# Kernel optimization log

Hardware: AMD Instinct MI355X
Metric: run time of the kernel (lower is better)

Reference implementation:

```python
import jax, jax.numpy as jnp
import numpy as np
import math

BATCH, NODES, IN_DIM = 8, 2048, 64
HEADS, OUT_DIM = 4, 32
D = HEADS * OUT_DIM
N_NEIGHBORS = 32


def setup_inputs() -> dict:
    key = jax.random.key(0)
    ks = jax.random.split(key, 6)
    s = lambda fan: 1.0 / np.sqrt(fan)
    return {
        "x": jax.random.normal(ks[0], (BATCH, NODES, IN_DIM), jnp.float32),
        "Wq": jax.random.normal(ks[1], (D, IN_DIM), jnp.float32) * s(IN_DIM),
        "bq": jnp.zeros((D,), jnp.float32),
        "Wk": jax.random.normal(ks[2], (D, IN_DIM), jnp.float32) * s(IN_DIM),
        "bk": jnp.zeros((D,), jnp.float32),
        "mlp_w": jax.random.normal(ks[3], (HEADS, HEADS), jnp.float32) * s(HEADS),
        "mlp_b": jnp.zeros((HEADS,), jnp.float32),
        "ln_g": jnp.ones((NODES,), jnp.float32),
        "ln_b": jnp.zeros((NODES,), jnp.float32),
    }


def _layernorm(x, g, b, eps=1e-5):
    m = x.mean(-1, keepdims=True)
    v = x.var(-1, keepdims=True)
    return (x - m) * jax.lax.rsqrt(v + eps) * g + b


def _forward(x, Wq, bq, Wk, bk, mlp_w, mlp_b, ln_g, ln_b):
    B, N, _ = x.shape
    # static graph branch (computed in the original forward, but its result is
    # never used in the returned adjacency -- kept for fidelity; DCE'd under jit)
    adj_static = jax.nn.softmax(
        jax.nn.relu(_layernorm(jnp.einsum('bnc,bmc->bnm', x, x), ln_g, ln_b)), axis=1)
    del adj_static

    q = x @ Wq.T + bq  # (B,N,D)
    k = x @ Wk.T + bk
    # (B,D,N) -> (B,H,d,N)
    q = q.transpose(0, 2, 1).reshape(B, HEADS, OUT_DIM, N)
    k = k.transpose(0, 2, 1).reshape(B, HEADS, OUT_DIM, N)
    q = q.transpose(0, 1, 3, 2)  # (B,H,N,d)

    # torch.split(query, chunk, dim=-1) splits q over out_dim, k over nodes; zip
    # truncates to the shorter list -> only min(nq,nk) chunks are processed.
    chunk = math.ceil(N / 2)
    nq = math.ceil(OUT_DIM / chunk)
    nk = math.ceil(N / chunk)
    inv_sqrt_d = jnp.float32(1.0 / math.sqrt(OUT_DIM))
    outs = []
    for i in range(min(nq, nk)):
        qc = q[..., i * chunk:(i + 1) * chunk]          # (B,H,N,dc)
        kc = k[..., i * chunk:(i + 1) * chunk]          # (B,H,d,Uc)
        a = jnp.einsum('bhnd,bhdu->bhnu', qc, kc) * inv_sqrt_d
        # dropout is identity in eval mode; soft-threshold with beta=0
        a = jnp.sign(a) * jax.nn.relu(jnp.abs(a))
        # 1x1 conv over head channels + relu, residual add
        a = jax.nn.relu(jnp.einsum('oh,bhnu->bonu', mlp_w, a)
                        + mlp_b[None, :, None, None]) + a
        outs.append(a)
    attn = jnp.concatenate(outs, axis=-1)               # (B,H,N,U)

    scores = attn.sum(axis=1)                           # (B,N,U)
    vals, idx = jax.lax.top_k(scores, N_NEIGHBORS)      # sorted, largest
    adj = jnp.zeros((B, N, N), x.dtype)
    bi = jnp.arange(B)[:, None, None]
    ni = jnp.arange(N)[None, :, None]
    return adj.at[bi, ni, idx].add(vals)


def reference(x, Wq, bq, Wk, bk, mlp_w, mlp_b, ln_g, ln_b):
    return _forward(x, Wq, bq, Wk, bk, mlp_w, mlp_b, ln_g, ln_b)
```

## Files before the change

kernel.cpp:

```cpp
#include <hip/hip_runtime.h>
#include <cstdint>
#include <cstddef>

#define BATCH 8
#define NODES 2048
#define IN_DIM 64
#define DTOT 128
#define NKEY 1024
#define LDK 136

typedef _Float16 half8v __attribute__((ext_vector_type(8)));
typedef float float4v __attribute__((ext_vector_type(4)));

__device__ __forceinline__ unsigned long long make_key(float v, int idx) {
    unsigned u = __float_as_uint(v);
    u = (u & 0x80000000u) ? ~u : (u | 0x80000000u);
    return ((unsigned long long)u << 32) | (unsigned)(1023 - idx);
}

__global__ __launch_bounds__(256) void proj_qk(
    const float* __restrict__ x, const float* __restrict__ Wq, const float* __restrict__ bq,
    const float* __restrict__ Wk, const float* __restrict__ bk,
    _Float16* __restrict__ qh, _Float16* __restrict__ ql,
    _Float16* __restrict__ kh, _Float16* __restrict__ kl)
{
    __shared__ float xs[64 * 68];
    __shared__ float wsh[64 * 68];

    const int t = threadIdx.x;
    const int blk = blockIdx.x;
    const int b = blk / 96;
    const int idx = blk - b * 96;

    const float* W; const float* bias;
    _Float16* oh; _Float16* ol;
    int nbase, cbase; size_t orow;
    if (idx < 64) {
        int nt = idx >> 1, ct = idx & 1;
        nbase = nt * 64; cbase = ct * 64;
        W = Wq; bias = bq; oh = qh; ol = ql;
        orow = (size_t)(b * NODES + nbase);
    } else {
        int i2 = idx - 64;
        int nt = i2 >> 1, ct = i2 & 1;
        nbase = nt * 64; cbase = ct * 64;
        W = Wk; bias = bk; oh = kh; ol = kl;
        orow = (size_t)(b * NKEY + nbase);
    }

    #pragma unroll
    for (int rep = 0; rep < 4; ++rep) {
        int f = rep * 256 + t;
        int r = f >> 4, d4 = f & 15;
        float4 xv = *(const float4*)(x + ((size_t)(b * NODES + nbase + r)) * IN_DIM + d4 * 4);
        *(float4*)(xs + r * 68 + d4 * 4) = xv;
        float4 wv = *(const float4*)(W + (size_t)(cbase + r) * IN_DIM + d4 * 4);
        *(float4*)(wsh + r * 68 + d4 * 4) = wv;
    }
    __syncthreads();

    const int w = t >> 6, l = t & 63;
    const int n_sel = w * 4 + (l >> 4);
    const int ul = l & 15;

    float acc[4][4];
    #pragma unroll
    for (int i = 0; i < 4; ++i)
        #pragma unroll
        for (int j = 0; j < 4; ++j) acc[i][j] = 0.f;

    #pragma unroll
    for (int d4 = 0; d4 < 16; ++d4) {
        float4 xv[4], wv[4];
        #pragma unroll
        for (int i = 0; i < 4; ++i)
            xv[i] = *(const float4*)(xs + (n_sel * 4 + i) * 68 + d4 * 4);
        #pragma unroll
        for (int j = 0; j < 4; ++j)
            wv[j] = *(const float4*)(wsh + (j * 16 + ul) * 68 + d4 * 4);
        #pragma unroll
        for (int i = 0; i < 4; ++i)
            #pragma unroll
            for (int j = 0; j < 4; ++j)
                acc[i][j] += xv[i].x * wv[j].x + xv[i].y * wv[j].y +
                             xv[i].z * wv[j].z + xv[i].w * wv[j].w;
    }

    #pragma unroll
    for (int j = 0; j < 4; ++j) {
        float bv = bias[cbase + j * 16 + ul];
        #pragma unroll
        for (int i = 0; i < 4; ++i) {
            float a = acc[i][j] + bv;
            _Float16 hi = (_Float16)a;
            size_t p = (orow + n_sel * 4 + i) * DTOT + cbase + j * 16 + ul;
            oh[p] = hi;
            ol[p] = (_Float16)(a - (float)hi);
        }
    }
}

__global__ __launch_bounds__(256, 4) void scores_mfma(
    const _Float16* __restrict__ qh, const _Float16* __restrict__ ql,
    const _Float16* __restrict__ kh, const _Float16* __restrict__ kl,
    const float* __restrict__ mlpw, const float* __restrict__ mlpb,
    float* __restrict__ adj)
{
    __shared__ _Float16 khs[64 * LDK];
    __shared__ _Float16 kls[64 * LDK];

    const int t = threadIdx.x;
    const int blk = blockIdx.x;
    const int b = blk >> 9;
    const int rem = blk & 511;
    const int nb = (rem >> 4) * 64;
    const int ub = (rem & 15) * 64;

    const int w = t >> 6, l = t & 63;
    const int quad = l >> 4, lane16 = l & 15;

    const size_t arow = (size_t)(b * NODES + nb + w * 16 + lane16);
    half8v Ah[4], Al[4];
    #pragma unroll
    for (int h = 0; h < 4; ++h) {
        Ah[h] = *(const half8v*)(qh + arow * DTOT + h * 32 + quad * 8);
        Al[h] = *(const half8v*)(ql + arow * DTOT + h * 32 + quad * 8);
    }

    #pragma unroll
    for (int rep = 0; rep < 4; ++rep) {
        int f = rep * 256 + t;
        int r = f >> 4, c = f & 15;
        size_t src = ((size_t)(b * NKEY + ub + r)) * DTOT + c * 8;
        *(half8v*)(&khs[r * LDK + c * 8]) = *(const half8v*)(kh + src);
        *(half8v*)(&kls[r * LDK + c * 8]) = *(const half8v*)(kl + src);
    }
    __syncthreads();

    float mw[4][4], mb4[4];
    #pragma unroll
    for (int o = 0; o < 4; ++o) {
        mb4[o] = mlpb[o];
        #pragma unroll
        for (int h = 0; h < 4; ++h) mw[o][h] = mlpw[o * 4 + h];
    }
    const float INV = 0.17677669529663687f;

    #pragma unroll
    for (int ut = 0; ut < 4; ++ut) {
        half8v Bh[4], Bl[4];
        #pragma unroll
        for (int h = 0; h < 4; ++h) {
            Bh[h] = *(const half8v*)(&khs[(ut * 16 + lane16) * LDK + h * 32 + quad * 8]);
            Bl[h] = *(const half8v*)(&kls[(ut * 16 + lane16) * LDK + h * 32 + quad * 8]);
        }
        float4v C[4];
        #pragma unroll
        for (int h = 0; h < 4; ++h) {
            float4v c = {0.f, 0.f, 0.f, 0.f};
            c = __builtin_amdgcn_mfma_f32_16x16x32_f16(Ah[h], Bh[h], c, 0, 0, 0);
            c = __builtin_amdgcn_mfma_f32_16x16x32_f16(Ah[h], Bl[h], c, 0, 0, 0);
            c = __builtin_amdgcn_mfma_f32_16x16x32_f16(Al[h], Bh[h], c, 0, 0, 0);
            C[h] = c;
        }
        #pragma unroll
        for (int r = 0; r < 4; ++r) {
            float a0 = C[0][r] * INV, a1 = C[1][r] * INV;
            float a2 = C[2][r] * INV, a3 = C[3][r] * INV;
            float ssum = a0 + a1 + a2 + a3;
            #pragma unroll
            for (int o = 0; o < 4; ++o) {
                float to = mw[o][0] * a0 + mw[o][1] * a1 + mw[o][2] * a2 + mw[o][3] * a3 + mb4[o];
                ssum += fmaxf(to, 0.f);
            }
            const size_t rowp = ((size_t)(b * NODES + nb + w * 16 + quad * 4 + r)) * NODES + NKEY;
            adj[rowp + ub + ut * 16 + lane16] = ssum;
        }
    }
}

__global__ __launch_bounds__(256) void topk_write(float* __restrict__ adj)
{
    __shared__ float scrow[4][1024];
    __shared__ unsigned long long cand[4][64];
    __shared__ float maxb[4][64];

    const int t = threadIdx.x;
    const int blk = blockIdx.x;
    const int b = blk >> 9;
    const int r0 = (blk & 511) * 4;
    const int w = t >> 6, l = t & 63;

    const int n = r0 + w;
    float* rowptr = adj + ((size_t)(b * NODES + n)) * NODES;
    const float4* S4 = (const float4*)(rowptr + NKEY);

    float4 vv[4];
    #pragma unroll
    for (int jj = 0; jj < 4; ++jj) vv[jj] = S4[jj * 64 + l];

    float m = vv[0].x;
    #pragma unroll
    for (int jj = 0; jj < 4; ++jj) {
        m = fmaxf(m, vv[jj].x); m = fmaxf(m, vv[jj].y);
        m = fmaxf(m, vv[jj].z); m = fmaxf(m, vv[jj].w);
    }

    maxb[w][l] = m;
    __builtin_amdgcn_wave_barrier();
    int r = 0;
    #pragma unroll
    for (int j = 0; j < 64; ++j) r += (maxb[w][j] > m) ? 1 : 0;
    float sel = (r <= 31) ? m : 3.4e38f;
    #pragma unroll
    for (int off = 1; off < 64; off <<= 1)
        sel = fminf(sel, __shfl_xor(sel, off, 64));
    const float T = sel;

    cand[w][l] = 0ull;
    __builtin_amdgcn_wave_barrier();
    int total = 0;
    #pragma unroll
    for (int jj = 0; jj < 4; ++jj) {
        #pragma unroll
        for (int e = 0; e < 4; ++e) {
            float v = (e == 0) ? vv[jj].x : (e == 1) ? vv[jj].y : (e == 2) ? vv[jj].z : vv[jj].w;
            bool p = (v >= T);
            unsigned long long msk = __ballot(p);
            if (p) {
                int pos = total + __popcll(msk & ((1ull << l) - 1ull));
                if (pos < 64) cand[w][pos] = make_key(v, jj * 256 + l * 4 + e);
            }
            total += (int)__popcll(msk);
        }
    }
    __builtin_amdgcn_wave_barrier();

    bool win = false; float wval = 0.f; int widx = 0;
    if (total <= 64) {
        unsigned long long key = cand[w][l];
        int r2 = 0;
        #pragma unroll
        for (int j = 0; j < 64; ++j) r2 += (cand[w][j] > key) ? 1 : 0;
        if (key != 0ull && r2 < 32) {
            win = true;
            unsigned hi = (unsigned)(key >> 32);
            wval = __uint_as_float((hi & 0x80000000u) ? (hi & 0x7fffffffu) : ~hi);
            widx = 1023 - (int)(key & 0xffffffffu);
        }
    } else {
        float vals[16];
        #pragma unroll
        for (int jj = 0; jj < 4; ++jj) {
            vals[jj * 4 + 0] = vv[jj].x; vals[jj * 4 + 1] = vv[jj].y;
            vals[jj * 4 + 2] = vv[jj].z; vals[jj * 4 + 3] = vv[jj].w;
        }
        float selv = 0.f; int seli = 0;
        #pragma unroll 1
        for (int it = 0; it < 32; ++it) {
            float bv = -3.4e38f; int bi = 0x7fffffff;
            #pragma unroll
            for (int s = 0; s < 16; ++s) {
                int idx = (s >> 2) * 256 + l * 4 + (s & 3);
                if (vals[s] > bv) { bv = vals[s]; bi = idx; }
            }
            #pragma unroll
            for (int off = 1; off < 64; off <<= 1) {
                float ov = __shfl_xor(bv, off, 64);
                int oi = __shfl_xor(bi, off, 64);
                if (ov > bv || (ov == bv && oi < bi)) { bv = ov; bi = oi; }
            }
            if (l == it) { selv = bv; seli = bi; }
            if (((bi >> 2) & 63) == l) {
                int slot = ((bi >> 8) << 2) + (bi & 3);
                #pragma unroll
                for (int s = 0; s < 16; ++s) if (s == slot) vals[s] = -3.4e38f;
            }
        }
        if (l < 32) { win = true; wval = selv; widx = seli; }
    }

    __builtin_amdgcn_wave_barrier();
    #pragma unroll
    for (int jj = 0; jj < 16; ++jj) scrow[w][l + (jj << 6)] = 0.f;
    __builtin_amdgcn_wave_barrier();
    if (win) scrow[w][widx] = wval;
    __builtin_amdgcn_wave_barrier();

    #pragma unroll
    for (int jj = 0; jj < 8; ++jj) {
        int c4 = jj * 64 + l;
        float4 val;
        if (c4 < 256) val = *(const float4*)(&scrow[w][c4 * 4]);
        else          val = make_float4(0.f, 0.f, 0.f, 0.f);
        *(float4*)(rowptr + c4 * 4) = val;
    }
}

extern "C" void kernel_launch(void* const* d_in, const int* in_sizes, int n_in,
                              void* d_out, int out_size, void* d_ws, size_t ws_size,
                              hipStream_t stream) {
    const float* x    = (const float*)d_in[0];
    const float* Wq   = (const float*)d_in[1];
    const float* bq   = (const float*)d_in[2];
    const float* Wk   = (const float*)d_in[3];
    const float* bk   = (const float*)d_in[4];
    const float* mlpw = (const float*)d_in[5];
    const float* mlpb = (const float*)d_in[6];

    _Float16* qh = (_Float16*)d_ws;
    _Float16* ql = qh + (size_t)BATCH * NODES * DTOT;
    _Float16* kh = ql + (size_t)BATCH * NODES * DTOT;
    _Float16* kl = kh + (size_t)BATCH * NKEY * DTOT;
    float* adj = (float*)d_out;

    proj_qk<<<dim3(BATCH * 96), dim3(256), 0, stream>>>(x, Wq, bq, Wk, bk, qh, ql, kh, kl);
    scores_mfma<<<dim3(BATCH * 512), dim3(256), 0, stream>>>(qh, ql, kh, kl, mlpw, mlpb, adj);
    topk_write<<<dim3(BATCH * 512), dim3(256), 0, stream>>>(adj);
}
```

Baseline: 191.1 us.

## Fuse score computation with top-k selection, keeping score rows in shared memory

Merges the MFMA score kernel and the top-k/write kernel into one. Each block computes a 16x1024 score tile into LDS and runs top-k on it directly, so the intermediate scores are no longer written to and re-read from the output buffer in global memory. Q/K are stored in an MFMA-fragment layout so each lane loads its fragment with one contiguous vector load, and K is read straight from global/L2 with no LDS staging. The cost is a large LDS footprint (about 66 KB) with launch bounds of 2 blocks per SM, only 1024 blocks, and every block re-reading all of K.

```diff
diff --git a/kernel.cpp b/kernel.cpp
--- a/kernel.cpp
+++ b/kernel.cpp
@@ -7,7 +7,9 @@
 #define IN_DIM 64
 #define DTOT 128
 #define NKEY 1024
-#define LDK 136
+#define QGROUPS 128
+#define KGROUPS 64
+#define SROW 1028
 
 typedef _Float16 half8v __attribute__((ext_vector_type(8)));
 typedef float float4v __attribute__((ext_vector_type(4)));
@@ -21,8 +23,8 @@
 __global__ __launch_bounds__(256) void proj_qk(
     const float* __restrict__ x, const float* __restrict__ Wq, const float* __restrict__ bq,
     const float* __restrict__ Wk, const float* __restrict__ bk,
-    _Float16* __restrict__ qh, _Float16* __restrict__ ql,
-    _Float16* __restrict__ kh, _Float16* __restrict__ kl)
+    _Float16* __restrict__ qfh, _Float16* __restrict__ qfl,
+    _Float16* __restrict__ kfh, _Float16* __restrict__ kfl)
 {
     __shared__ float xs[64 * 68];
     __shared__ float wsh[64 * 68];
@@ -34,19 +36,20 @@
 
     const float* W; const float* bias;
     _Float16* oh; _Float16* ol;
-    int nbase, cbase; size_t orow;
+    int nbase, cbase; size_t gbase;
     if (idx < 64) {
         int nt = idx >> 1, ct = idx & 1;
         nbase = nt * 64; cbase = ct * 64;
-        W = Wq; bias = bq; oh = qh; ol = ql;
-        orow = (size_t)(b * NODES + nbase);
+        W = Wq; bias = bq; oh = qfh; ol = qfl;
+        gbase = (size_t)b * QGROUPS + (nbase >> 4);
     } else {
         int i2 = idx - 64;
         int nt = i2 >> 1, ct = i2 & 1;
         nbase = nt * 64; cbase = ct * 64;
-        W = Wk; bias = bk; oh = kh; ol = kl;
-        orow = (size_t)(b * NKEY + nbase);
-    }
+        W = Wk; bias = bk; oh = kfh; ol = kfl;
+        gbase = (size_t)b * KGROUPS + (nbase >> 4);
+    }
+    const int hbase = cbase >> 5;
 
     #pragma unroll
     for (int rep = 0; rep < 4; ++rep) {
@@ -85,57 +88,63 @@
                 acc[i][j] += xv[i].x * wv[j].x + xv[i].y * wv[j].y +
                              xv[i].z * wv[j].z + xv[i].w * wv[j].w;
     }
+    __syncthreads();
 
     #pragma unroll
     for (int j = 0; j < 4; ++j) {
         float bv = bias[cbase + j * 16 + ul];
         #pragma unroll
-        for (int i = 0; i < 4; ++i) {
-            float a = acc[i][j] + bv;
-            _Float16 hi = (_Float16)a;
-            size_t p = (orow + n_sel * 4 + i) * DTOT + cbase + j * 16 + ul;
-            oh[p] = hi;
-            ol[p] = (_Float16)(a - (float)hi);
-        }
+        for (int i = 0; i < 4; ++i)
+            xs[(n_sel * 4 + i) * 68 + j * 16 + ul] = acc[i][j] + bv;
+    }
+    __syncthreads();
+
+    #pragma unroll
+    for (int rep = 0; rep < 2; ++rep) {
+        int u = rep * 256 + t;
+        int g = u >> 7, hh = (u >> 6) & 1, lf = u & 63;
+        const float* src = xs + (g * 16 + (lf & 15)) * 68 + hh * 32 + (lf >> 4) * 8;
+        float4 f0 = *(const float4*)src;
+        float4 f1 = *(const float4*)(src + 4);
+        float tmp[8] = {f0.x, f0.y, f0.z, f0.w, f1.x, f1.y, f1.z, f1.w};
+        half8v hv, lv;
+        #pragma unroll
+        for (int e = 0; e < 8; ++e) {
+            _Float16 hi = (_Float16)tmp[e];
+            hv[e] = hi;
+            lv[e] = (_Float16)(tmp[e] - (float)hi);
+        }
+        size_t dst = ((gbase + g) * 4 + hbase + hh) * (size_t)512 + lf * 8;
+        *(half8v*)(oh + dst) = hv;
+        *(half8v*)(ol + dst) = lv;
     }
 }
 
-__global__ __launch_bounds__(256, 4) void scores_mfma(
-    const _Float16* __restrict__ qh, const _Float16* __restrict__ ql,
-    const _Float16* __restrict__ kh, const _Float16* __restrict__ kl,
+__global__ __launch_bounds__(256, 2) void scores_topk(
+    const _Float16* __restrict__ qfh, const _Float16* __restrict__ qfl,
+    const _Float16* __restrict__ kfh, const _Float16* __restrict__ kfl,
     const float* __restrict__ mlpw, const float* __restrict__ mlpb,
     float* __restrict__ adj)
 {
-    __shared__ _Float16 khs[64 * LDK];
-    __shared__ _Float16 kls[64 * LDK];
+    __shared__ float sc[16 * SROW];
+    __shared__ unsigned long long cand[4][64];
+    __shared__ float maxb[4][64];
 
     const int t = threadIdx.x;
     const int blk = blockIdx.x;
-    const int b = blk >> 9;
-    const int rem = blk & 511;
-    const int nb = (rem >> 4) * 64;
-    const int ub = (rem & 15) * 64;
+    const int b = blk >> 7;
+    const int gq = blk & 127;
 
     const int w = t >> 6, l = t & 63;
     const int quad = l >> 4, lane16 = l & 15;
 
-    const size_t arow = (size_t)(b * NODES + nb + w * 16 + lane16);
     half8v Ah[4], Al[4];
     #pragma unroll
     for (int h = 0; h < 4; ++h) {
-        Ah[h] = *(const half8v*)(qh + arow * DTOT + h * 32 + quad * 8);
-        Al[h] = *(const half8v*)(ql + arow * DTOT + h * 32 + quad * 8);
-    }
-
-    #pragma unroll
-    for (int rep = 0; rep < 4; ++rep) {
-        int f = rep * 256 + t;
-        int r = f >> 4, c = f & 15;
-        size_t src = ((size_t)(b * NKEY + ub + r)) * DTOT + c * 8;
-        *(half8v*)(&khs[r * LDK + c * 8]) = *(const half8v*)(kh + src);
-        *(half8v*)(&kls[r * LDK + c * 8]) = *(const half8v*)(kl + src);
-    }
-    __syncthreads();
+        size_t a = (((size_t)b * QGROUPS + gq) * 4 + h) * 512 + l * 8;
+        Ah[h] = *(const half8v*)(qfh + a);
+        Al[h] = *(const half8v*)(qfl + a);
+    }
 
     float mw[4][4], mb4[4];
     #pragma unroll
@@ -146,13 +155,15 @@
     }
     const float INV = 0.17677669529663687f;
 
-    #pragma unroll
-    for (int ut = 0; ut < 4; ++ut) {
+    #pragma unroll 2
+    for (int i = 0; i < 16; ++i) {
+        const int g = w * 16 + i;
         half8v Bh[4], Bl[4];
         #pragma unroll
         for (int h = 0; h < 4; ++h) {
-            Bh[h] = *(const half8v*)(&khs[(ut * 16 + lane16) * LDK + h * 32 + quad * 8]);
-            Bl[h] = *(const half8v*)(&kls[(ut * 16 + lane16) * LDK + h * 32 + quad * 8]);
+            size_t a = (((size_t)b * KGROUPS + g) * 4 + h) * 512 + l * 8;
+            Bh[h] = *(const half8v*)(kfh + a);
+            Bl[h] = *(const half8v*)(kfl + a);
         }
         float4v C[4];
         #pragma unroll
@@ -173,127 +184,116 @@
                 float to = mw[o][0] * a0 + mw[o][1] * a1 + mw[o][2] * a2 + mw[o][3] * a3 + mb4[o];
                 ssum += fmaxf(to, 0.f);
             }
-            const size_t rowp = ((size_t)(b * NODES + nb + w * 16 + quad * 4 + r)) * NODES + NKEY;
-            adj[rowp + ub + ut * 16 + lane16] = ssum;
-        }
-    }
-}
-
-__global__ __launch_bounds__(256) void topk_write(float* __restrict__ adj)
-{
-    __shared__ float scrow[4][1024];
-    __shared__ unsigned long long cand[4][64];
-    __shared__ float maxb[4][64];
-
-    const int t = threadIdx.x;
-    const int blk = blockIdx.x;
-    const int b = blk >> 9;
-    const int r0 = (blk & 511) * 4;
-    const int w = t >> 6, l = t & 63;
-
-    const int n = r0 + w;
-    float* rowptr = adj + ((size_t)(b * NODES + n)) * NODES;
-    const float4* S4 = (const float4*)(rowptr + NKEY);
-
-    float4 vv[4];
-    #pragma unroll
-    for (int jj = 0; jj < 4; ++jj) vv[jj] = S4[jj * 64 + l];
-
-    float m = vv[0].x;
-    #pragma unroll
-    for (int jj = 0; jj < 4; ++jj) {
-        m = fmaxf(m, vv[jj].x); m = fmaxf(m, vv[jj].y);
-        m = fmaxf(m, vv[jj].z); m = fmaxf(m, vv[jj].w);
-    }
-
-    maxb[w][l] = m;
-    __builtin_amdgcn_wave_barrier();
-    int r = 0;
-    #pragma unroll
-    for (int j = 0; j < 64; ++j) r += (maxb[w][j] > m) ? 1 : 0;
-    float sel = (r <= 31) ? m : 3.4e38f;
-    #pragma unroll
-    for (int off = 1; off < 64; off <<= 1)
-        sel = fminf(sel, __shfl_xor(sel, off, 64));
-    const float T = sel;
-
-    cand[w][l] = 0ull;
-    __builtin_amdgcn_wave_barrier();
-    int total = 0;
-    #pragma unroll
-    for (int jj = 0; jj < 4; ++jj) {
-        #pragma unroll
-        for (int e = 0; e < 4; ++e) {
-            float v = (e == 0) ? vv[jj].x : (e == 1) ? vv[jj].y : (e == 2) ? vv[jj].z : vv[jj].w;
-            bool p = (v >= T);
-            unsigned long long msk = __ballot(p);
-            if (p) {
-                int pos = total + __popcll(msk & ((1ull << l) - 1ull));
-                if (pos < 64) cand[w][pos] = make_key(v, jj * 256 + l * 4 + e);
-            }
-            total += (int)__popcll(msk);
-        }
-    }
-    __builtin_amdgcn_wave_barrier();
-
-    bool win = false; float wval = 0.f; int widx = 0;
-    if (total <= 64) {
-        unsigned long long key = cand[w][l];
-        int r2 = 0;
-        #pragma unroll
-        for (int j = 0; j < 64; ++j) r2 += (cand[w][j] > key) ? 1 : 0;
-        if (key != 0ull && r2 < 32) {
-            win = true;
-            unsigned hi = (unsigned)(key >> 32);
-            wval = __uint_as_float((hi & 0x80000000u) ? (hi & 0x7fffffffu) : ~hi);
-            widx = 1023 - (int)(key & 0xffffffffu);
-        }
-    } else {
-        float vals[16];
+            sc[(quad * 4 + r) * SROW + g * 16 + lane16] = ssum;
+        }
+    }
+    __syncthreads();
+
+    for (int rr = 0; rr < 4; ++rr) {
+        const int row = rr * 4 + w;
+        float* R = sc + row * SROW;
+
+        float4 vv[4];
+        #pragma unroll
+        for (int jj = 0; jj < 4; ++jj) vv[jj] = *(const float4*)(R + jj * 256 + l * 4);
+
+        float m = vv[0].x;
         #pragma unroll
         for (int jj = 0; jj < 4; ++jj) {
-            vals[jj * 4 + 0] = vv[jj].x; vals[jj * 4 + 1] = vv[jj].y;
-            vals[jj * 4 + 2] = vv[jj].z; vals[jj * 4 + 3] = vv[jj].w;
-        }
-        float selv = 0.f; int seli = 0;
-        #pragma unroll 1
-        for (int it = 0; it < 32; ++it) {
-            float bv = -3.4e38f; int bi = 0x7fffffff;
-            #pragma unroll
-            for (int s = 0; s < 16; ++s) {
-                int idx = (s >> 2) * 256 + l * 4 + (s & 3);
-                if (vals[s] > bv) { bv = vals[s]; bi = idx; }
-            }
-            #pragma unroll
-            for (int off = 1; off < 64; off <<= 1) {
-                float ov = __shfl_xor(bv, off, 64);
-                int oi = __shfl_xor(bi, off, 64);
-                if (ov > bv || (ov == bv && oi < bi)) { bv = ov; bi = oi; }
-            }
-            if (l == it) { selv = bv; seli = bi; }
-            if (((bi >> 2) & 63) == l) {
-                int slot = ((bi >> 8) << 2) + (bi & 3);
+            m = fmaxf(m, vv[jj].x); m = fmaxf(m, vv[jj].y);
+            m = fmaxf(m, vv[jj].z); m = fmaxf(m, vv[jj].w);
+        }
+
+        maxb[w][l] = m;
+        __builtin_amdgcn_wave_barrier();
+        int rk = 0;
+        #pragma unroll
+        for (int j = 0; j < 64; ++j) rk += (maxb[w][j] > m) ? 1 : 0;
+        float sel = (rk <= 31) ? m : 3.4e38f;
+        #pragma unroll
+        for (int off = 1; off < 64; off <<= 1)
+            sel = fminf(sel, __shfl_xor(sel, off, 64));
+        const float T = sel;
+
+        cand[w][l] = 0ull;
+        __builtin_amdgcn_wave_barrier();
+        int total = 0;
+        #pragma unroll
+        for (int jj = 0; jj < 4; ++jj) {
+            #pragma unroll
+            for (int e = 0; e < 4; ++e) {
+                float v = (e == 0) ? vv[jj].x : (e == 1) ? vv[jj].y : (e == 2) ? vv[jj].z : vv[jj].w;
+                bool p = (v >= T);
+                unsigned long long msk = __ballot(p);
+                if (p) {
+                    int pos = total + __popcll(msk & ((1ull << l) - 1ull));
+                    if (pos < 64) cand[w][pos] = make_key(v, jj * 256 + l * 4 + e);
+                }
+                total += (int)__popcll(msk);
+            }
+        }
+        __builtin_amdgcn_wave_barrier();
+
+        bool win = false; float wval = 0.f; int widx = 0;
+        if (total <= 64) {
+            unsigned long long key = cand[w][l];
+            int r2 = 0;
+            #pragma unroll
+            for (int j = 0; j < 64; ++j) r2 += (cand[w][j] > key) ? 1 : 0;
+            if (key != 0ull && r2 < 32) {
+                win = true;
+                unsigned hi = (unsigned)(key >> 32);
+                wval = __uint_as_float((hi & 0x80000000u) ? (hi & 0x7fffffffu) : ~hi);
+                widx = 1023 - (int)(key & 0xffffffffu);
+            }
+        } else {
+            float vals[16];
+            #pragma unroll
+            for (int jj = 0; jj < 4; ++jj) {
+                vals[jj * 4 + 0] = vv[jj].x; vals[jj * 4 + 1] = vv[jj].y;
+                vals[jj * 4 + 2] = vv[jj].z; vals[jj * 4 + 3] = vv[jj].w;
+            }
+            float selv = 0.f; int seli = 0;
+            #pragma unroll 1
+            for (int it = 0; it < 32; ++it) {
+                float bv = -3.4e38f; int bi = 0x7fffffff;
                 #pragma unroll
-                for (int s = 0; s < 16; ++s) if (s == slot) vals[s] = -3.4e38f;
-            }
-        }
-        if (l < 32) { win = true; wval = selv; widx = seli; }
-    }
-
-    __builtin_amdgcn_wave_barrier();
-    #pragma unroll
-    for (int jj = 0; jj < 16; ++jj) scrow[w][l + (jj << 6)] = 0.f;
-    __builtin_amdgcn_wave_barrier();
-    if (win) scrow[w][widx] = wval;
-    __builtin_amdgcn_wave_barrier();
-
-    #pragma unroll
-    for (int jj = 0; jj < 8; ++jj) {
-        int c4 = jj * 64 + l;
-        float4 val;
-        if (c4 < 256) val = *(const float4*)(&scrow[w][c4 * 4]);
-        else          val = make_float4(0.f, 0.f, 0.f, 0.f);
-        *(float4*)(rowptr + c4 * 4) = val;
+                for (int s = 0; s < 16; ++s) {
+                    int idx2 = (s >> 2) * 256 + l * 4 + (s & 3);
+                    if (vals[s] > bv) { bv = vals[s]; bi = idx2; }
+                }
+                #pragma unroll
+                for (int off = 1; off < 64; off <<= 1) {
+                    float ov = __shfl_xor(bv, off, 64);
+                    int oi = __shfl_xor(bi, off, 64);
+                    if (ov > bv || (ov == bv && oi < bi)) { bv = ov; bi = oi; }
+                }
+                if (l == it) { selv = bv; seli = bi; }
+                if (((bi >> 2) & 63) == l) {
+                    int slot = ((bi >> 8) << 2) + (bi & 3);
+                    #pragma unroll
+                    for (int s = 0; s < 16; ++s) if (s == slot) vals[s] = -3.4e38f;
+                }
+            }
+            if (l < 32) { win = true; wval = selv; widx = seli; }
+        }
+
+        __builtin_amdgcn_wave_barrier();
+        #pragma unroll
+        for (int jj = 0; jj < 16; ++jj) R[l + (jj << 6)] = 0.f;
+        __builtin_amdgcn_wave_barrier();
+        if (win) R[widx] = wval;
+        __builtin_amdgcn_wave_barrier();
+
+        float* rowptr = adj + ((size_t)(b * NODES + gq * 16 + row)) * NODES;
+        #pragma unroll
+        for (int jj = 0; jj < 8; ++jj) {
+            int c4 = jj * 64 + l;
+            float4 val;
+            if (c4 < 256) val = *(const float4*)(R + c4 * 4);
+            else          val = make_float4(0.f, 0.f, 0.f, 0.f);
+            *(float4*)(rowptr + c4 * 4) = val;
+        }
     }
 }
 
@@ -308,13 +308,12 @@
     const float* mlpw = (const float*)d_in[5];
     const float* mlpb = (const float*)d_in[6];
 
-    _Float16* qh = (_Float16*)d_ws;
-    _Float16* ql = qh + (size_t)BATCH * NODES * DTOT;
-    _Float16* kh = ql + (size_t)BATCH * NODES * DTOT;
-    _Float16* kl = kh + (size_t)BATCH * NKEY * DTOT;
+    _Float16* qfh = (_Float16*)d_ws;
+    _Float16* qfl = qfh + (size_t)BATCH * NODES * DTOT;
+    _Float16* kfh = qfl + (size_t)BATCH * NODES * DTOT;
+    _Float16* kfl = kfh + (size_t)BATCH * NKEY * DTOT;
     float* adj = (float*)d_out;
 
-    proj_qk<<<dim3(BATCH * 96), dim3(256), 0, stream>>>(x, Wq, bq, Wk, bk, qh, ql, kh, kl);
-    scores_mfma<<<dim3(BATCH * 512), dim3(256), 0, stream>>>(qh, ql, kh, kl, mlpw, mlpb, adj);
-    topk_write<<<dim3(BATCH * 512), dim3(256), 0, stream>>>(adj);
+    proj_qk<<<dim3(BATCH * 96), dim3(256), 0, stream>>>(x, Wq, bq, Wk, bk, qfh, qfl, kfh, kfl);
+    scores_topk<<<dim3(BATCH * QGROUPS), dim3(256), 0, stream>>>(qfh, qfl, kfh, kfl, mlpw, mlpb, adj);
 }
```

New measurement: 196.7 us. 1.03x slower.
